# Performance work log

Hardware: AMD Instinct MI355X
Metric: run time of the kernel (lower is better)

## Reference

```python
import jax, jax.numpy as jnp
import numpy as np

PATCH_SIZE = 24
ALPHA = 0.2  # LeakyReLU negative slope


def setup_inputs() -> dict:
    key = jax.random.key(0)
    k_x, k_adj, k_w, k_wc = jax.random.split(key, 4)
    B, T, N, Cin, Cout = 2, 96, 64, 16, 32
    x = jax.random.normal(k_x, (B, T, N, Cin), dtype=jnp.float32)
    adj = jax.random.uniform(k_adj, (N, N), dtype=jnp.float32)  # weighted adjacency in [0,1)
    # xavier_uniform with gain=1.414 on (Cin, Cout)
    limit = 1.414 * float(np.sqrt(6.0 / (Cin + Cout)))
    W = jax.random.uniform(k_w, (Cin, Cout), dtype=jnp.float32, minval=-limit, maxval=limit)
    W_c = jax.random.uniform(k_wc, (Cout,), dtype=jnp.float32, minval=-0.1, maxval=0.1)
    return {"x": x, "adj": adj, "W": W, "W_c": W_c}


def reference(x, adj, W, W_c):
    B, T, N, Cin = x.shape
    P = PATCH_SIZE
    NP = T // P
    Cout = W.shape[1]
    # torch.view semantics == row-major jnp.reshape (faithful, even though it mixes axes)
    x_patched = x.reshape(B, NP, N, P, Cin)
    h = x_patched @ W  # (B, NP, N, P, Cout)
    # vectorized over patches: per-patch outer product over nodes
    e = jnp.einsum('bsipc,bsjpc->bsijpc', h, h)  # (B, NP, N, N, P, Cout)
    e = jnp.where(e >= 0, e, ALPHA * e)  # LeakyReLU
    e = e * adj[None, None, :, :, None, None]
    e = jax.nn.softmax(e, axis=-1)  # softmax over channel dim (as in original)
    # torch.stack(list, dim=4) of (b,i,j,p,c) over patch index -> (B,N,N,P,NP,C)
    e = jnp.transpose(e, (0, 2, 3, 4, 1, 5))
    attention = e.reshape(B, N, N, T, Cout)  # (B, N, N, T, Cout)
    # h_patched.permute(0,2,1,3,4).reshape(B,N,T,C)
    h_flat = jnp.transpose(h, (0, 2, 1, 3, 4)).reshape(B, N, T, Cout)
    # einsum('bnqtc,bntc->bntc') == sum over q then elementwise multiply
    h_prime = attention.sum(axis=2) * h_flat
    return attention, jax.nn.elu(h_prime)
```

## Files before the change

### kernel.cpp

```cpp
#include <hip/hip_runtime.h>
#include <math.h>

#define Bq 2
#define Tq 96
#define Nq 64
#define CIN 16
#define COUT 32
#define PATCH 24
#define NPq 4
#define JC 4
#define JPER (Nq / JC)
#define ATT_SIZE (Bq * Nq * Nq * Tq * COUT)
#define HP_SIZE (Bq * Nq * Tq * COUT)
#define H_ROWS (Bq * NPq * Nq * PATCH)
#define SLAB (Nq * PATCH * COUT)

typedef float f4 __attribute__((ext_vector_type(4)));

__global__ __launch_bounds__(256) void h_gemm_kernel(
    const float* __restrict__ x, const float* __restrict__ W,
    float* __restrict__ h) {
    __shared__ float Wl[CIN * COUT];
    __shared__ float xs[8 * CIN];
    int tid = threadIdx.x;
    Wl[tid]       = W[tid];
    Wl[tid + 256] = W[tid + 256];
    if (tid < 8 * CIN) xs[tid] = x[blockIdx.x * (8 * CIN) + tid];
    __syncthreads();
    int rl = tid >> 5;
    int c  = tid & 31;
    float acc = 0.f;
#pragma unroll
    for (int k = 0; k < CIN; ++k)
        acc += xs[rl * CIN + k] * Wl[k * COUT + c];
    h[blockIdx.x * 256 + tid] = acc;
}

__global__ __launch_bounds__(768) void att_kernel(
    const float* __restrict__ h, const float* __restrict__ adj,
    float* __restrict__ att, float* __restrict__ part) {
    const int bi = blockIdx.x;
    const int jc = bi & 3;
    const int i  = (bi >> 2) & 63;
    const int b  = bi >> 8;
    const int j0 = jc * JPER;
    const int tid = threadIdx.x;
    const int c0 = (tid & 7) * 4;
    const int t  = tid >> 3;
    const int s  = t & 3;
    const int p  = t >> 2;

    __shared__ float adjrow[JPER];
    if (tid < JPER) adjrow[tid] = adj[i * Nq + j0 + tid];
    __syncthreads();

    const float* hslab = h + (size_t)(b * NPq + s) * SLAB;
    const f4 hi = *(const f4*)(hslab + (i * PATCH + p) * COUT + c0);

    f4 acc = {0.f, 0.f, 0.f, 0.f};
    size_t outbase = ((size_t)((b * Nq + i) * Nq + j0) * Tq + t) * COUT + c0;
    const size_t jstride = (size_t)Tq * COUT;

#pragma unroll 4
    for (int jj = 0; jj < JPER; ++jj) {
        const f4 hj = *(const f4*)(hslab + ((j0 + jj) * PATCH + p) * COUT + c0);
        const float aj = adjrow[jj];

        f4 e = hi * hj;
        e.x = fmaxf(e.x, 0.2f * e.x) * aj;
        e.y = fmaxf(e.y, 0.2f * e.y) * aj;
        e.z = fmaxf(e.z, 0.2f * e.z) * aj;
        e.w = fmaxf(e.w, 0.2f * e.w) * aj;

        f4 ex;
        ex.x = __expf(e.x); ex.y = __expf(e.y);
        ex.z = __expf(e.z); ex.w = __expf(e.w);
        float sm = (ex.x + ex.y) + (ex.z + ex.w);
#pragma unroll
        for (int d = 1; d < 8; d <<= 1) sm += __shfl_xor(sm, d);
        const float inv = __builtin_amdgcn_rcpf(sm);
        f4 a = ex * inv;
        acc += a;
        __builtin_nontemporal_store(a, (f4*)(att + outbase + (size_t)jj * jstride));
    }

    float* pp = part + (size_t)jc * HP_SIZE
                     + ((size_t)((b * Nq + i) * Tq + t)) * COUT + c0;
    *(f4*)pp = acc;
}

__global__ __launch_bounds__(256) void hprime_kernel(
    const float* __restrict__ part, const float* __restrict__ h,
    float* __restrict__ hprime) {
    const int vid  = blockIdx.x * 256 + threadIdx.x;
    const int base = vid * 4;
    const int c  = base & 31;
    const int t  = (base >> 5) % Tq;
    const int bi = base / (COUT * Tq);
    const int i  = bi & 63;
    const int b  = bi >> 6;

    f4 a0 = *(const f4*)(part + base);
    f4 a1 = *(const f4*)(part + base + HP_SIZE);
    f4 a2 = *(const f4*)(part + base + 2 * HP_SIZE);
    f4 a3 = *(const f4*)(part + base + 3 * HP_SIZE);
    f4 asum = (a0 + a1) + (a2 + a3);

    const int s2 = t / PATCH;
    const int p2 = t % PATCH;
    const f4 hv = *(const f4*)(h + (size_t)((b * NPq + s2) * Nq + i) * (PATCH * COUT)
                                 + p2 * COUT + c);
    f4 v = asum * hv;
    v.x = v.x >= 0.f ? v.x : expm1f(v.x);
    v.y = v.y >= 0.f ? v.y : expm1f(v.y);
    v.z = v.z >= 0.f ? v.z : expm1f(v.z);
    v.w = v.w >= 0.f ? v.w : expm1f(v.w);
    *(f4*)(hprime + base) = v;
}

extern "C" void kernel_launch(void* const* d_in, const int* in_sizes, int n_in,
                              void* d_out, int out_size, void* d_ws, size_t ws_size,
                              hipStream_t stream) {
    (void)in_sizes; (void)n_in; (void)out_size; (void)ws_size;
    const float* x   = (const float*)d_in[0];
    const float* adj = (const float*)d_in[1];
    const float* W   = (const float*)d_in[2];

    float* h    = (float*)d_ws;
    float* part = (float*)d_ws + H_ROWS * COUT;
    float* att  = (float*)d_out;
    float* hp   = (float*)d_out + ATT_SIZE;

    hipLaunchKernelGGL(h_gemm_kernel, dim3(H_ROWS / 8), dim3(256), 0, stream,
                       x, W, h);
    hipLaunchKernelGGL(att_kernel, dim3(Bq * Nq * JC), dim3(768), 0, stream,
                       h, adj, att, part);
    hipLaunchKernelGGL(hprime_kernel, dim3(HP_SIZE / 4 / 256), dim3(256), 0, stream,
                       part, h, hp);
}
```

Before: 35.08 us.

## Give each thread all 32 channels to drop softmax shuffles in attention kernel

The attention kernel now assigns one thread per (t, j-half) holding all 32 channels, so the channel softmax sum is computed in registers instead of with cross-lane shuffles. Blocks shrink from 768 to 192 threads, and the two j-halves are combined through shared memory before the partial sums are written. Stores change from nontemporal to regular, and each thread writes 128 contiguous bytes per j instead of lanes writing coalesced 16-byte pieces. The costs are higher register pressure, fewer threads per block, and a less coalesced store pattern on a kernel dominated by output writes.

```diff
diff --git a/kernel.cpp b/kernel.cpp
--- a/kernel.cpp
+++ b/kernel.cpp
@@ -9,7 +9,6 @@
 #define PATCH 24
 #define NPq 4
 #define JC 4
-#define JPER (Nq / JC)
 #define ATT_SIZE (Bq * Nq * Nq * Tq * COUT)
 #define HP_SIZE (Bq * Nq * Tq * COUT)
 #define H_ROWS (Bq * NPq * Nq * PATCH)
@@ -36,57 +35,82 @@
     h[blockIdx.x * 256 + tid] = acc;
 }
 
-__global__ __launch_bounds__(768) void att_kernel(
+__global__ __launch_bounds__(192) void att_kernel(
     const float* __restrict__ h, const float* __restrict__ adj,
     float* __restrict__ att, float* __restrict__ part) {
     const int bi = blockIdx.x;
     const int jc = bi & 3;
     const int i  = (bi >> 2) & 63;
     const int b  = bi >> 8;
-    const int j0 = jc * JPER;
-    const int tid = threadIdx.x;
-    const int c0 = (tid & 7) * 4;
-    const int t  = tid >> 3;
-    const int s  = t & 3;
-    const int p  = t >> 2;
+    const int tid  = threadIdx.x;
+    const int t    = tid % 96;
+    const int jsub = tid / 96;
+    const int s = t & 3;
+    const int p = t >> 2;
+    const int j0 = jc * 16 + jsub * 8;
 
-    __shared__ float adjrow[JPER];
-    if (tid < JPER) adjrow[tid] = adj[i * Nq + j0 + tid];
+    __shared__ float adjrow[16];
+    __shared__ float red[96 * 32];
+    if (tid < 16) adjrow[tid] = adj[i * Nq + jc * 16 + tid];
     __syncthreads();
 
-    const float* hslab = h + (size_t)(b * NPq + s) * SLAB;
-    const f4 hi = *(const f4*)(hslab + (i * PATCH + p) * COUT + c0);
+    const float* hb = h + (size_t)(b * NPq + s) * SLAB;
+    f4 hi[8], acc[8];
+#pragma unroll
+    for (int q = 0; q < 8; ++q) {
+        hi[q]  = *(const f4*)(hb + (i * PATCH + p) * COUT + q * 4);
+        acc[q] = (f4){0.f, 0.f, 0.f, 0.f};
+    }
 
-    f4 acc = {0.f, 0.f, 0.f, 0.f};
-    size_t outbase = ((size_t)((b * Nq + i) * Nq + j0) * Tq + t) * COUT + c0;
+    size_t outbase = ((size_t)((b * Nq + i) * Nq + j0) * Tq + t) * COUT;
     const size_t jstride = (size_t)Tq * COUT;
 
-#pragma unroll 4
-    for (int jj = 0; jj < JPER; ++jj) {
-        const f4 hj = *(const f4*)(hslab + ((j0 + jj) * PATCH + p) * COUT + c0);
-        const float aj = adjrow[jj];
+#pragma unroll
+    for (int jj = 0; jj < 8; ++jj) {
+        const float aj = adjrow[jsub * 8 + jj];
+        const float* hjp = hb + ((j0 + jj) * PATCH + p) * COUT;
 
-        f4 e = hi * hj;
-        e.x = fmaxf(e.x, 0.2f * e.x) * aj;
-        e.y = fmaxf(e.y, 0.2f * e.y) * aj;
-        e.z = fmaxf(e.z, 0.2f * e.z) * aj;
-        e.w = fmaxf(e.w, 0.2f * e.w) * aj;
+        f4 ex[8];
+#pragma unroll
+        for (int q = 0; q < 8; ++q) {
+            f4 e = hi[q] * (*(const f4*)(hjp + q * 4));
+            e.x = fmaxf(e.x, 0.2f * e.x) * aj;
+            e.y = fmaxf(e.y, 0.2f * e.y) * aj;
+            e.z = fmaxf(e.z, 0.2f * e.z) * aj;
+            e.w = fmaxf(e.w, 0.2f * e.w) * aj;
+            ex[q].x = __expf(e.x); ex[q].y = __expf(e.y);
+            ex[q].z = __expf(e.z); ex[q].w = __expf(e.w);
+        }
+        f4 s0 = (ex[0] + ex[1]) + (ex[2] + ex[3]);
+        f4 s1 = (ex[4] + ex[5]) + (ex[6] + ex[7]);
+        f4 sv = s0 + s1;
+        const float sm = (sv.x + sv.y) + (sv.z + sv.w);
+        const float inv = __builtin_amdgcn_rcpf(sm);
 
-        f4 ex;
-        ex.x = __expf(e.x); ex.y = __expf(e.y);
-        ex.z = __expf(e.z); ex.w = __expf(e.w);
-        float sm = (ex.x + ex.y) + (ex.z + ex.w);
+        float* op = att + outbase + (size_t)jj * jstride;
 #pragma unroll
-        for (int d = 1; d < 8; d <<= 1) sm += __shfl_xor(sm, d);
-        const float inv = __builtin_amdgcn_rcpf(sm);
-        f4 a = ex * inv;
-        acc += a;
-        __builtin_nontemporal_store(a, (f4*)(att + outbase + (size_t)jj * jstride));
+        for (int q = 0; q < 8; ++q) {
+            f4 a = ex[q] * inv;
+            acc[q] += a;
+            *(f4*)(op + q * 4) = a;
+        }
     }
 
-    float* pp = part + (size_t)jc * HP_SIZE
-                     + ((size_t)((b * Nq + i) * Tq + t)) * COUT + c0;
-    *(f4*)pp = acc;
+    if (jsub == 1) {
+#pragma unroll
+        for (int q = 0; q < 8; ++q)
+            *(f4*)(&red[t * COUT + q * 4]) = acc[q];
+    }
+    __syncthreads();
+    if (jsub == 0) {
+        float* pp = part + (size_t)jc * HP_SIZE
+                         + ((size_t)((b * Nq + i) * Tq + t)) * COUT;
+#pragma unroll
+        for (int q = 0; q < 8; ++q) {
+            f4 r = *(const f4*)(&red[t * COUT + q * 4]);
+            *(f4*)(pp + q * 4) = acc[q] + r;
+        }
+    }
 }
 
 __global__ __launch_bounds__(256) void hprime_kernel(
@@ -133,7 +157,7 @@
 
     hipLaunchKernelGGL(h_gemm_kernel, dim3(H_ROWS / 8), dim3(256), 0, stream,
                        x, W, h);
-    hipLaunchKernelGGL(att_kernel, dim3(Bq * Nq * JC), dim3(768), 0, stream,
+    hipLaunchKernelGGL(att_kernel, dim3(Bq * Nq * JC), dim3(192), 0, stream,
                        h, adj, att, part);
     hipLaunchKernelGGL(hprime_kernel, dim3(HP_SIZE / 4 / 256), dim3(256), 0, stream,
                        part, h, hp);
```

Measured after the change: 56.86 us. 62.1% more time.
